# Performance work log

Hardware: AMD Instinct MI355X
Metric: run time of the kernel (lower is better)

## Reference

```python
import jax, jax.numpy as jnp
import numpy as np
from jax import lax

VOCAB = 32000
D = 256      # d_model
N = 16       # n_neurons
NL = 6       # n_layers
DS = 16      # d_state
DC = 4       # d_conv
DI = 512     # d_inner = expand * d_model
DTR = 16     # dt_rank = ceil(D/16)
NH = 4       # attention heads
HD = D // NH
B, L = 1, 128


def setup_inputs() -> dict:
    key = jax.random.key(0)
    ks = list(jax.random.split(key, 32))
    it = iter(ks)

    def rn(shape, scale):
        return jax.random.normal(next(it), shape, jnp.float32) * scale

    p = {}
    p["x"] = jax.random.randint(next(it), (B, L), 0, VOCAB, dtype=jnp.int32)
    p["embedding"] = rn((VOCAB, D), 0.02)
    p["norm1_w"] = jnp.ones((NL, D)); p["norm1_b"] = jnp.zeros((NL, D))
    p["norm2_w"] = jnp.ones((NL, D)); p["norm2_b"] = jnp.zeros((NL, D))
    # Mamba params (stacked over layers)
    p["in_proj_w"] = rn((NL, 2 * DI, D), D ** -0.5)
    p["conv_w"] = rn((NL, DI, DC), DC ** -0.5)
    p["conv_b"] = jnp.zeros((NL, DI))
    p["x_proj_w"] = rn((NL, DTR + 2 * DS, DI), DI ** -0.5)
    p["dt_proj_w"] = rn((NL, DI, DTR), DTR ** -0.5)
    dt0 = jax.random.uniform(next(it), (NL, DI), jnp.float32, 1e-3, 1e-1)
    p["dt_proj_b"] = jnp.log(jnp.expm1(dt0))  # inverse softplus init
    p["A_log"] = jnp.log(jnp.tile(jnp.arange(1.0, DS + 1.0, dtype=jnp.float32), (NL, DI, 1)))
    p["skip_D"] = jnp.ones((NL, DI))
    p["out_proj_w"] = rn((NL, D, DI), DI ** -0.5)
    # cross-neuron MHA params
    p["attn_in_w"] = rn((NL, 3 * D, D), D ** -0.5)
    p["attn_in_b"] = jnp.zeros((NL, 3 * D))
    p["attn_out_w"] = rn((NL, D, D), D ** -0.5)
    p["attn_out_b"] = jnp.zeros((NL, D))
    p["norm_f_w"] = jnp.ones((D,)); p["norm_f_b"] = jnp.zeros((D,))
    p["head_b"] = jnp.zeros((VOCAB,))
    return p


def _ln(x, w, b):
    m = x.mean(-1, keepdims=True)
    v = ((x - m) ** 2).mean(-1, keepdims=True)
    return (x - m) * lax.rsqrt(v + 1e-5) * w + b


def _mamba(x, ipw, cw, cb, xpw, dpw, dpb, alog, dskip, opw):
    # x: (BN, L, D)
    BN, Ls, _ = x.shape
    xz = x @ ipw.T                       # (BN, L, 2*DI)
    u, z = xz[..., :DI], xz[..., DI:]
    # depthwise causal conv1d, kernel DC, left-pad DC-1
    uc = lax.conv_general_dilated(
        u.swapaxes(1, 2), cw[:, None, :], (1,), [(DC - 1, 0)],
        dimension_numbers=("NCH", "OIH", "NCH"), feature_group_count=DI)
    u = jax.nn.silu(uc + cb[None, :, None]).swapaxes(1, 2)  # (BN, L, DI)
    xdbl = u @ xpw.T                     # (BN, L, DTR+2*DS)
    dt = jax.nn.softplus(xdbl[..., :DTR] @ dpw.T + dpb)     # (BN, L, DI)
    Bm = xdbl[..., DTR:DTR + DS]
    Cm = xdbl[..., DTR + DS:]
    A = -jnp.exp(alog)                   # (DI, DS)

    def step(h, ins):
        dt_t, b_t, c_t, u_t = ins        # (BN,DI) (BN,DS) (BN,DS) (BN,DI)
        h = jnp.exp(dt_t[..., None] * A) * h + (dt_t * u_t)[..., None] * b_t[:, None, :]
        return h, jnp.einsum("bds,bs->bd", h, c_t)

    h0 = jnp.zeros((BN, DI, DS), x.dtype)
    _, ys = lax.scan(step, h0, (dt.swapaxes(0, 1), Bm.swapaxes(0, 1),
                                Cm.swapaxes(0, 1), u.swapaxes(0, 1)))
    y = ys.swapaxes(0, 1) + u * dskip
    return (y * jax.nn.silu(z)) @ opw.T


def _mha(x, iw, ib, ow, ob):
    # x: (B*L, N, D); self-attention across neurons
    Bq, S, _ = x.shape
    qkv = x @ iw.T + ib
    q, k, v = jnp.split(qkv, 3, axis=-1)
    q = q.reshape(Bq, S, NH, HD); k = k.reshape(Bq, S, NH, HD); v = v.reshape(Bq, S, NH, HD)
    att = jax.nn.softmax(jnp.einsum("bqhd,bkhd->bhqk", q, k) / np.float32(np.sqrt(HD)), axis=-1)
    o = jnp.einsum("bhqk,bkhd->bqhd", att, v).reshape(Bq, S, D)
    return o @ ow.T + ob


def reference(x, embedding, norm1_w, norm1_b, norm2_w, norm2_b, in_proj_w, conv_w,
              conv_b, x_proj_w, dt_proj_w, dt_proj_b, A_log, skip_D, out_proj_w,
              attn_in_w, attn_in_b, attn_out_w, attn_out_b, norm_f_w, norm_f_b, head_b):
    Bb, Ll = x.shape
    h = embedding[x]                                             # (B, L, D)
    h = jnp.broadcast_to(h[:, None], (Bb, N, Ll, D)).reshape(Bb * N, Ll, D)
    for i in range(NL):
        h = h + _mamba(_ln(h, norm1_w[i], norm1_b[i]), in_proj_w[i], conv_w[i],
                       conv_b[i], x_proj_w[i], dt_proj_w[i], dt_proj_b[i],
                       A_log[i], skip_D[i], out_proj_w[i])
        xc = _ln(h, norm2_w[i], norm2_b[i]).reshape(Bb, N, Ll, D)
        xc = xc.transpose(0, 2, 1, 3).reshape(Bb * Ll, N, D)
        co = _mha(xc, attn_in_w[i], attn_in_b[i], attn_out_w[i], attn_out_b[i])
        h = h + co.reshape(Bb, Ll, N, D).transpose(0, 2, 1, 3).reshape(Bb * N, Ll, D)
    h = h.reshape(Bb, N, Ll, D).mean(axis=1)                     # avg over neurons
    return _ln(h, norm_f_w, norm_f_b) @ embedding.T + head_b     # tied head
```

## Files before the change

### kernel.cpp

```cpp
#include <hip/hip_runtime.h>

constexpr int SEQ    = 128;
constexpr int NVOCAB = 32000;

constexpr size_t O_HA = 0;
constexpr size_t O_HB = O_HA + (size_t)SEQ*256;
constexpr size_t O_U  = O_HB + (size_t)SEQ*256;
constexpr size_t O_DT = O_U  + (size_t)SEQ*512;
constexpr size_t O_ZS = O_DT + (size_t)SEQ*512;
constexpr size_t O_BC = O_ZS + (size_t)SEQ*512;
constexpr size_t O_YG = O_BC + (size_t)SEQ*32;
constexpr size_t O_AH = O_YG + (size_t)SEQ*512;
constexpr size_t O_WC = O_AH + (size_t)SEQ*256;
constexpr size_t O_BB = O_WC + (size_t)6*256*256;

__device__ __forceinline__ float wsum(float p) {
    #pragma unroll
    for (int m = 1; m < 64; m <<= 1) p += __shfl_xor(p, m);
    return p;
}
__device__ __forceinline__ float dot4(float4 a, float4 b) {
    return a.x*b.x + a.y*b.y + a.z*b.z + a.w*b.w;
}

__global__ __launch_bounds__(256) void combo_kernel(
    const float* __restrict__ aiw, const float* __restrict__ aib,
    const float* __restrict__ aow, const float* __restrict__ aob,
    float* __restrict__ wc, float* __restrict__ bc)
{
    const int l   = blockIdx.x >> 4;
    const int c0  = (blockIdx.x & 15) * 16;
    const int tid = threadIdx.x;
    const int c   = c0 + (tid >> 4);
    const int k0  = (tid & 15) * 16;
    const float* av = aiw + (size_t)l*768*256 + (size_t)512*256;
    const float* ab = aib + l*768 + 512;
    const float* ow = aow + (size_t)l*256*256;
    const float* ob = aob + l*256;

    float4 acc[4] = {};
    for (int j0 = 0; j0 < 256; j0 += 4) {
        float4 a4 = *(const float4*)&ow[(size_t)c*256 + j0];
        #pragma unroll
        for (int jj = 0; jj < 4; ++jj) {
            float aj = (&a4.x)[jj];
            const float* wrow = av + (size_t)(j0+jj)*256 + k0;
            #pragma unroll
            for (int q = 0; q < 4; ++q) {
                float4 w4 = *(const float4*)(wrow + q*4);
                acc[q].x += aj*w4.x; acc[q].y += aj*w4.y;
                acc[q].z += aj*w4.z; acc[q].w += aj*w4.w;
            }
        }
    }
    float* wout = wc + (size_t)l*256*256 + (size_t)c*256 + k0;
    #pragma unroll
    for (int q = 0; q < 4; ++q) *(float4*)(wout + q*4) = acc[q];

    if ((tid & 15) == 0) {
        float b = ob[c];
        for (int j0 = 0; j0 < 256; j0 += 4) {
            float4 a4 = *(const float4*)&ow[(size_t)c*256 + j0];
            float4 b4 = *(const float4*)&ab[j0];
            b += a4.x*b4.x + a4.y*b4.y + a4.z*b4.z + a4.w*b4.w;
        }
        bc[l*256 + c] = b;
    }
}

template<int MR, int KK, int S>
__device__ __forceinline__ void gemm3(
    const float* __restrict__ Wg, const float* __restrict__ A, int AS,
    float* __restrict__ dest, int DS,
    const float* __restrict__ addsrc, int ASS, const float* __restrict__ bias)
{
    constexpr int NST = KK / (4 * S);
    const int tid = threadIdx.x;
    const int tq  = tid & (S - 1);
    const int c0  = (tid / S) * 2;
    const float* Wp0 = Wg + (size_t)c0*KK + tq*4;
    const float* Wp1 = Wp0 + KK;

    float acc0[MR], acc1[MR];
    #pragma unroll
    for (int r = 0; r < MR; ++r) { acc0[r] = 0.f; acc1[r] = 0.f; }

    float4 wa0 = *(const float4*)(Wp0);
    float4 wa1 = *(const float4*)(Wp1);
    float4 wb0 = *(const float4*)(Wp0 + 4*S);
    float4 wb1 = *(const float4*)(Wp1 + 4*S);

    #pragma unroll 1
    for (int st = 0; st < NST; st += 2) {
        float4 na0, na1, nb0, nb1;
        const bool pa = (st + 2 < NST);
        const bool pb = (st + 3 < NST);
        if (pa) { na0 = *(const float4*)(Wp0 + (st+2)*4*S);
                  na1 = *(const float4*)(Wp1 + (st+2)*4*S); }
        if (pb) { nb0 = *(const float4*)(Wp0 + (st+3)*4*S);
                  nb1 = *(const float4*)(Wp1 + (st+3)*4*S); }
        const int k0 = st*4*S + tq*4;
        #pragma unroll
        for (int r = 0; r < MR; ++r) {
            float4 a = *(const float4*)&A[r*AS + k0];
            acc0[r] += dot4(a, wa0);
            acc1[r] += dot4(a, wa1);
        }
        const int k1 = k0 + 4*S;
        #pragma unroll
        for (int r = 0; r < MR; ++r) {
            float4 a = *(const float4*)&A[r*AS + k1];
            acc0[r] += dot4(a, wb0);
            acc1[r] += dot4(a, wb1);
        }
        if (pa) { wa0 = na0; wa1 = na1; }
        if (pb) { wb0 = nb0; wb1 = nb1; }
    }
    #pragma unroll
    for (int m = 1; m < S; m <<= 1) {
        #pragma unroll
        for (int r = 0; r < MR; ++r) {
            acc0[r] += __shfl_xor(acc0[r], m);
            acc1[r] += __shfl_xor(acc1[r], m);
        }
    }
    if (tq == 0) {
        #pragma unroll
        for (int r = 0; r < MR; ++r) {
            float ox = acc0[r], oy = acc1[r];
            if (bias) { ox += bias[c0]; oy += bias[c0+1]; }
            if (addsrc) {
                float2 s = *(const float2*)&addsrc[r*ASS + c0];
                ox += s.x; oy += s.y;
            }
            float2 o; o.x = ox; o.y = oy;
            *(float2*)&dest[r*DS + c0] = o;
        }
    }
}

__device__ __forceinline__ void ln_row(const float* __restrict__ src, float* __restrict__ dst,
                                       const float* __restrict__ w, const float* __restrict__ b)
{
    int lane = threadIdx.x & 63;
    float4 x = *(const float4*)&src[lane*4];
    float sm = wsum(x.x + x.y + x.z + x.w);
    float mean = sm * (1.0f/256.0f);
    float d0 = x.x-mean, d1 = x.y-mean, d2 = x.z-mean, d3 = x.w-mean;
    float var = wsum(d0*d0 + d1*d1 + d2*d2 + d3*d3) * (1.0f/256.0f);
    float rstd = rsqrtf(var + 1e-5f);
    float4 ww = *(const float4*)&w[lane*4];
    float4 bb = *(const float4*)&b[lane*4];
    float4 o;
    o.x = d0*rstd*ww.x + bb.x;
    o.y = d1*rstd*ww.y + bb.y;
    o.z = d2*rstd*ww.z + bb.z;
    o.w = d3*rstd*ww.w + bb.w;
    *(float4*)&dst[lane*4] = o;
}

__global__ __launch_bounds__(1024, 4) void rowk_kernel(
    const int* __restrict__ x, const float* __restrict__ emb,
    const float* __restrict__ n1w_l, const float* __restrict__ n1b_l,
    const float* __restrict__ n2w_l, const float* __restrict__ n2b_l,
    const float* __restrict__ ipw_l, const float* __restrict__ cw_l, const float* __restrict__ cb_l,
    const float* __restrict__ xpw_l, const float* __restrict__ dpw_l, const float* __restrict__ dpb_l,
    const float* __restrict__ opw_l, const float* __restrict__ wc_l, const float* __restrict__ bc_l,
    const float* __restrict__ nfw, const float* __restrict__ nfb,
    const float* __restrict__ hin, float* __restrict__ hout,
    const float* __restrict__ ygv, float* __restrict__ uv, float* __restrict__ dtv,
    float* __restrict__ zsv, float* __restrict__ bcv, float* __restrict__ AH,
    int li)
{
    __shared__ float SM[6336];
    float* hP  = SM;
    float* h1  = SM + 1056;
    float* sLN = SM + 2112;
    float* sAX = SM + 3168;
    float* zR  = SM + 5248;
    float* suR = SM + 5760;
    float* sxR = SM + 6272;

    const int r = blockIdx.x;
    const int tid = threadIdx.x;
    const int lane = tid & 63, wv = tid >> 6;
    int rr[4];
    #pragma unroll
    for (int j = 0; j < 4; ++j) { int v = r - 3 + j; rr[j] = v < 0 ? 0 : v; }

    {
        int hr = tid >> 8, hc = tid & 255;
        if (li <= 1) hP[hr*264 + hc] = emb[(size_t)x[rr[hr]]*256 + hc];
        else         hP[hr*264 + hc] = hin[rr[hr]*256 + hc];
    }
    if (li >= 1) {
        int yr = tid >> 9, yc = tid & 511;
        sAX[yr*520 + yc]     = ygv[rr[yr]*512 + yc];
        sAX[(2+yr)*520 + yc] = ygv[rr[2+yr]*512 + yc];
    }
    __syncthreads();

    float* hC = hP;
    if (li >= 1) {
        gemm3<4,512,8>(opw_l, sAX, 520, h1, 264, hP, 264, nullptr);
        __syncthreads();
        if (wv < 4) ln_row(h1 + wv*264, sLN + wv*264, n2w_l, n2b_l);
        __syncthreads();
        gemm3<4,256,8>(wc_l, sLN, 264, h1, 264, h1, 264, bc_l);
        __syncthreads();
        hC = h1;
        if (tid < 256) hout[r*256 + tid] = h1[3*264 + tid];
        if (li == 6) {
            if (tid < 256) {
                float v = h1[3*264 + tid];
                float s = wsum(v);
                float q = wsum(v*v);
                if (lane == 0) { sxR[wv] = s; sxR[8 + wv] = q; }
            }
            __syncthreads();
            if (tid < 256) {
                float v = h1[3*264 + tid];
                float mean = (sxR[0]+sxR[1]+sxR[2]+sxR[3]) * (1.0f/256.0f);
                float var  = (sxR[8]+sxR[9]+sxR[10]+sxR[11]) * (1.0f/256.0f) - mean*mean;
                float rstd = rsqrtf(var + 1e-5f);
                AH[r*256 + tid] = (v - mean)*rstd*nfw[tid] + nfb[tid];
            }
            return;
        }
    }

    if (wv < 4) ln_row(hC + wv*264, sLN + wv*264, n1w_l, n1b_l);
    __syncthreads();
    gemm3<4,256,4>(ipw_l,                   sLN,         264, sAX, 520, nullptr, 0, nullptr);
    gemm3<1,256,4>(ipw_l + (size_t)512*256, sLN + 3*264, 264, zR,  512, nullptr, 0, nullptr);
    __syncthreads();

    if (tid < 512) {
        int d = tid;
        float4 c4 = *(const float4*)&cw_l[d*4];
        float acc = cb_l[d];
        if (r >= 3) acc += sAX[d]        * c4.x;
        if (r >= 2) acc += sAX[520 + d]  * c4.y;
        if (r >= 1) acc += sAX[1040 + d] * c4.z;
        acc += sAX[1560 + d] * c4.w;
        float sg = acc / (1.0f + __expf(-acc));
        suR[d] = sg;
        uv[r*512 + d] = sg;
        float z = zR[d];
        zsv[r*512 + d] = z / (1.0f + __expf(-z));
    }
    __syncthreads();

    {
        float4 a0 = *(const float4*)&suR[lane*4];
        float4 a1 = *(const float4*)&suR[256 + lane*4];
        float p[3];
        #pragma unroll
        for (int j = 0; j < 3; ++j) {
            int c = wv*3 + j;
            float4 q0 = *(const float4*)&xpw_l[(size_t)c*512 + lane*4];
            float4 q1 = *(const float4*)&xpw_l[(size_t)c*512 + 256 + lane*4];
            p[j] = dot4(a0, q0) + dot4(a1, q1);
        }
        #pragma unroll
        for (int m = 1; m < 64; m <<= 1) {
            #pragma unroll
            for (int j = 0; j < 3; ++j) p[j] += __shfl_xor(p[j], m);
        }
        if (lane == 0) {
            #pragma unroll
            for (int j = 0; j < 3; ++j) sxR[wv*3 + j] = p[j];
        }
    }
    __syncthreads();
    if (tid >= 16 && tid < 48) bcv[r*32 + tid - 16] = sxR[tid];

    if (tid < 512) {
        int d = tid;
        float4 sx0 = *(const float4*)&sxR[0];
        float4 sx1 = *(const float4*)&sxR[4];
        float4 sx2 = *(const float4*)&sxR[8];
        float4 sx3 = *(const float4*)&sxR[12];
        const float4* dp = (const float4*)&dpw_l[(size_t)d*16];
        float acc = dpb_l[d] + dot4(dp[0], sx0) + dot4(dp[1], sx1)
                             + dot4(dp[2], sx2) + dot4(dp[3], sx3);
        dtv[r*512 + d] = fmaxf(acc, 0.0f) + log1pf(__expf(-fabsf(acc)));
    }
}

__global__ __launch_bounds__(64) void scan_kernel(
    const float* __restrict__ dt, const float* __restrict__ u, const float* __restrict__ zs,
    const float* __restrict__ bcv,
    const float* __restrict__ alog_l, const float* __restrict__ dsk_l,
    float* __restrict__ yg)
{
    __shared__ float sdt[4*132];
    __shared__ float su2[4*132];
    __shared__ float sz2[4*132];
    __shared__ float sB [16*132];
    __shared__ float sC [16*132];
    const int tid = threadIdx.x;
    const int s  = tid & 15;
    const int dl = tid >> 4;
    const int d0 = blockIdx.x * 4;
    const int d  = d0 + dl;

    #pragma unroll
    for (int tt = 0; tt < 2; ++tt) {
        const int t = tid + tt*64;
        float4 q;
        q = *(const float4*)&dt[t*512 + d0];
        sdt[0*132+t]=q.x; sdt[1*132+t]=q.y; sdt[2*132+t]=q.z; sdt[3*132+t]=q.w;
        q = *(const float4*)&u[t*512 + d0];
        su2[0*132+t]=q.x; su2[1*132+t]=q.y; su2[2*132+t]=q.z; su2[3*132+t]=q.w;
        q = *(const float4*)&zs[t*512 + d0];
        sz2[0*132+t]=q.x; sz2[1*132+t]=q.y; sz2[2*132+t]=q.z; sz2[3*132+t]=q.w;
        float4 b0 = *(const float4*)&bcv[t*32 + 0];
        float4 b1 = *(const float4*)&bcv[t*32 + 4];
        float4 b2 = *(const float4*)&bcv[t*32 + 8];
        float4 b3 = *(const float4*)&bcv[t*32 + 12];
        sB[ 0*132+t]=b0.x; sB[ 1*132+t]=b0.y; sB[ 2*132+t]=b0.z; sB[ 3*132+t]=b0.w;
        sB[ 4*132+t]=b1.x; sB[ 5*132+t]=b1.y; sB[ 6*132+t]=b1.z; sB[ 7*132+t]=b1.w;
        sB[ 8*132+t]=b2.x; sB[ 9*132+t]=b2.y; sB[10*132+t]=b2.z; sB[11*132+t]=b2.w;
        sB[12*132+t]=b3.x; sB[13*132+t]=b3.y; sB[14*132+t]=b3.z; sB[15*132+t]=b3.w;
        float4 c0 = *(const float4*)&bcv[t*32 + 16];
        float4 c1 = *(const float4*)&bcv[t*32 + 20];
        float4 c2 = *(const float4*)&bcv[t*32 + 24];
        float4 c3 = *(const float4*)&bcv[t*32 + 28];
        sC[ 0*132+t]=c0.x; sC[ 1*132+t]=c0.y; sC[ 2*132+t]=c0.z; sC[ 3*132+t]=c0.w;
        sC[ 4*132+t]=c1.x; sC[ 5*132+t]=c1.y; sC[ 6*132+t]=c1.z; sC[ 7*132+t]=c1.w;
        sC[ 8*132+t]=c2.x; sC[ 9*132+t]=c2.y; sC[10*132+t]=c2.z; sC[11*132+t]=c2.w;
        sC[12*132+t]=c3.x; sC[13*132+t]=c3.y; sC[14*132+t]=c3.z; sC[15*132+t]=c3.w;
    }
    __syncthreads();

    const float a_ds = -__expf(alog_l[d*16 + s]);
    const float dskv = dsk_l[d];
    float hst = 0.0f;
    #pragma unroll 8
    for (int t = 0; t < SEQ; ++t) {
        float dtvv = sdt[dl*132 + t];
        float uvv  = su2[dl*132 + t];
        hst = __expf(dtvv * a_ds) * hst + dtvv * uvv * sB[s*132 + t];
        float p = hst * sC[s*132 + t];
        p += __shfl_xor(p, 1);
        p += __shfl_xor(p, 2);
        p += __shfl_xor(p, 4);
        p += __shfl_xor(p, 8);
        if (s == 0) yg[t*512 + d] = (p + uvv * dskv) * sz2[dl*132 + t];
    }
}

__global__ __launch_bounds__(256) void head_kernel(
    const float* __restrict__ AH, const float* __restrict__ emb,
    const float* __restrict__ hb, float* __restrict__ out)
{
    __shared__ float sA[32*132];
    __shared__ float sW[32*68];
    const int tid = threadIdx.x;
    const int c0  = blockIdx.x * 64;
    const int ar = tid >> 1;
    const int ak = (tid & 1) * 16;
    const int wc = tid & 63;
    const int wk = (tid >> 6) * 8;
    const int rg = tid >> 4;
    const int cg = tid & 15;

    const float* Ap = AH  + (size_t)ar*256 + ak;
    const float* Wp = emb + (size_t)(c0 + wc)*256 + wk;

    float4 ra0 = *(const float4*)(Ap + 0);
    float4 ra1 = *(const float4*)(Ap + 4);
    float4 ra2 = *(const float4*)(Ap + 8);
    float4 ra3 = *(const float4*)(Ap + 12);
    float4 rw0 = *(const float4*)(Wp + 0);
    float4 rw1 = *(const float4*)(Wp + 4);

    float acc[8][4] = {};

    for (int kc = 0; kc < 256; kc += 32) {
        if (kc) __syncthreads();
        sA[(ak+ 0)*132+ar]=ra0.x; sA[(ak+ 1)*132+ar]=ra0.y; sA[(ak+ 2)*132+ar]=ra0.z; sA[(ak+ 3)*132+ar]=ra0.w;
        sA[(ak+ 4)*132+ar]=ra1.x; sA[(ak+ 5)*132+ar]=ra1.y; sA[(ak+ 6)*132+ar]=ra1.z; sA[(ak+ 7)*132+ar]=ra1.w;
        sA[(ak+ 8)*132+ar]=ra2.x; sA[(ak+ 9)*132+ar]=ra2.y; sA[(ak+10)*132+ar]=ra2.z; sA[(ak+11)*132+ar]=ra2.w;
        sA[(ak+12)*132+ar]=ra3.x; sA[(ak+13)*132+ar]=ra3.y; sA[(ak+14)*132+ar]=ra3.z; sA[(ak+15)*132+ar]=ra3.w;
        sW[(wk+0)*68+wc]=rw0.x; sW[(wk+1)*68+wc]=rw0.y; sW[(wk+2)*68+wc]=rw0.z; sW[(wk+3)*68+wc]=rw0.w;
        sW[(wk+4)*68+wc]=rw1.x; sW[(wk+5)*68+wc]=rw1.y; sW[(wk+6)*68+wc]=rw1.z; sW[(wk+7)*68+wc]=rw1.w;
        __syncthreads();
        if (kc + 32 < 256) {
            ra0 = *(const float4*)(Ap + kc + 32);
            ra1 = *(const float4*)(Ap + kc + 36);
            ra2 = *(const float4*)(Ap + kc + 40);
            ra3 = *(const float4*)(Ap + kc + 44);
            rw0 = *(const float4*)(Wp + kc + 32);
            rw1 = *(const float4*)(Wp + kc + 36);
        }
        #pragma unroll
        for (int k = 0; k < 32; ++k) {
            float4 a0 = *(const float4*)&sA[k*132 + rg*8];
            float4 a1 = *(const float4*)&sA[k*132 + rg*8 + 4];
            float4 b  = *(const float4*)&sW[k*68  + cg*4];
            float av[8] = {a0.x,a0.y,a0.z,a0.w, a1.x,a1.y,a1.z,a1.w};
            #pragma unroll
            for (int i = 0; i < 8; ++i) {
                acc[i][0] += av[i]*b.x;
                acc[i][1] += av[i]*b.y;
                acc[i][2] += av[i]*b.z;
                acc[i][3] += av[i]*b.w;
            }
        }
    }

    const int c = c0 + cg*4;
    float4 h4 = *(const float4*)&hb[c];
    #pragma unroll
    for (int i = 0; i < 8; ++i) {
        int r = rg*8 + i;
        float4 o;
        o.x = acc[i][0] + h4.x;
        o.y = acc[i][1] + h4.y;
        o.z = acc[i][2] + h4.z;
        o.w = acc[i][3] + h4.w;
        *(float4*)&out[(size_t)r*NVOCAB + c] = o;
    }
}

extern "C" void kernel_launch(void* const* d_in, const int* in_sizes, int n_in,
                              void* d_out, int out_size, void* d_ws, size_t ws_size,
                              hipStream_t stream)
{
    const int*   xin = (const int*)d_in[0];
    const float* emb = (const float*)d_in[1];
    const float* n1w = (const float*)d_in[2];
    const float* n1b = (const float*)d_in[3];
    const float* n2w = (const float*)d_in[4];
    const float* n2b = (const float*)d_in[5];
    const float* ipw = (const float*)d_in[6];
    const float* cw  = (const float*)d_in[7];
    const float* cb  = (const float*)d_in[8];
    const float* xpw = (const float*)d_in[9];
    const float* dpw = (const float*)d_in[10];
    const float* dpb = (const float*)d_in[11];
    const float* alog= (const float*)d_in[12];
    const float* dsk = (const float*)d_in[13];
    const float* opw = (const float*)d_in[14];
    const float* aiw = (const float*)d_in[15];
    const float* aib = (const float*)d_in[16];
    const float* aow = (const float*)d_in[17];
    const float* aob = (const float*)d_in[18];
    const float* nfw = (const float*)d_in[19];
    const float* nfb = (const float*)d_in[20];
    const float* hb  = (const float*)d_in[21];
    float* ws  = (float*)d_ws;
    float* out = (float*)d_out;

    combo_kernel<<<96, 256, 0, stream>>>(aiw, aib, aow, aob, ws + O_WC, ws + O_BB);

    for (int i = 0; i <= 6; ++i) {
        int ka = i <= 5 ? i : 5;
        int kc = i >= 1 ? i - 1 : 0;
        const float* hin  = (i % 2 == 0) ? ws + O_HA : ws + O_HB;
        float*       hout = (i % 2 == 0) ? ws + O_HB : ws + O_HA;
        rowk_kernel<<<128, 1024, 0, stream>>>(
            xin, emb,
            n1w + ka*256, n1b + ka*256,
            n2w + kc*256, n2b + kc*256,
            ipw + (size_t)ka*1024*256, cw + (size_t)ka*512*4, cb + ka*512,
            xpw + (size_t)ka*48*512, dpw + (size_t)ka*512*16, dpb + ka*512,
            opw + (size_t)kc*256*512,
            ws + O_WC + (size_t)kc*256*256, ws + O_BB + kc*256,
            nfw, nfb,
            hin, hout,
            ws + O_YG, ws + O_U, ws + O_DT, ws + O_ZS, ws + O_BC, ws + O_AH,
            i);
        if (i <= 5)
            scan_kernel<<<128, 64, 0, stream>>>(
                ws + O_DT, ws + O_U, ws + O_ZS, ws + O_BC,
                alog + (size_t)i*512*16, dsk + i*512, ws + O_YG);
    }
    head_kernel<<<NVOCAB/64, 256, 0, stream>>>(ws + O_AH, emb, hb, out);
}
```

Before: 596.6 us.

## Tile the attention weight-combination GEMM through shared memory with register prefetch

```diff
diff --git a/kernel.cpp b/kernel.cpp
--- a/kernel.cpp
+++ b/kernel.cpp
@@ -28,41 +28,72 @@
     const float* __restrict__ aow, const float* __restrict__ aob,
     float* __restrict__ wc, float* __restrict__ bc)
 {
-    const int l   = blockIdx.x >> 4;
-    const int c0  = (blockIdx.x & 15) * 16;
+    __shared__ float sA[32*68];
+    __shared__ float sB[32*68];
+    const int l  = blockIdx.x >> 4;
+    const int t  = blockIdx.x & 15;
+    const int r0 = (t >> 2) * 64;
+    const int n0 = (t & 3) * 64;
     const int tid = threadIdx.x;
-    const int c   = c0 + (tid >> 4);
-    const int k0  = (tid & 15) * 16;
+
     const float* av = aiw + (size_t)l*768*256 + (size_t)512*256;
     const float* ab = aib + l*768 + 512;
     const float* ow = aow + (size_t)l*256*256;
     const float* ob = aob + l*256;
 
-    float4 acc[4] = {};
-    for (int j0 = 0; j0 < 256; j0 += 4) {
-        float4 a4 = *(const float4*)&ow[(size_t)c*256 + j0];
-        #pragma unroll
-        for (int jj = 0; jj < 4; ++jj) {
-            float aj = (&a4.x)[jj];
-            const float* wrow = av + (size_t)(j0+jj)*256 + k0;
-            #pragma unroll
-            for (int q = 0; q < 4; ++q) {
-                float4 w4 = *(const float4*)(wrow + q*4);
-                acc[q].x += aj*w4.x; acc[q].y += aj*w4.y;
-                acc[q].z += aj*w4.z; acc[q].w += aj*w4.w;
-            }
-        }
-    }
-    float* wout = wc + (size_t)l*256*256 + (size_t)c*256 + k0;
-    #pragma unroll
-    for (int q = 0; q < 4; ++q) *(float4*)(wout + q*4) = acc[q];
-
-    if ((tid & 15) == 0) {
+    const int ar = tid & 63, ah = (tid >> 6) * 8;
+    const int bk = tid >> 3, bn = (tid & 7) * 8;
+    const float* Ap = ow + (size_t)(r0 + ar)*256 + ah;
+    const float* Bp = av + (size_t)bk*256 + n0 + bn;
+
+    const int rg = tid >> 4, cg = tid & 15;
+
+    float4 ra0 = *(const float4*)(Ap);
+    float4 ra1 = *(const float4*)(Ap + 4);
+    float4 rb0 = *(const float4*)(Bp);
+    float4 rb1 = *(const float4*)(Bp + 4);
+
+    float acc[4][4] = {};
+
+    for (int kc = 0; kc < 256; kc += 32) {
+        if (kc) __syncthreads();
+        sA[(ah+0)*68+ar]=ra0.x; sA[(ah+1)*68+ar]=ra0.y; sA[(ah+2)*68+ar]=ra0.z; sA[(ah+3)*68+ar]=ra0.w;
+        sA[(ah+4)*68+ar]=ra1.x; sA[(ah+5)*68+ar]=ra1.y; sA[(ah+6)*68+ar]=ra1.z; sA[(ah+7)*68+ar]=ra1.w;
+        *(float4*)&sB[bk*68+bn]   = rb0;
+        *(float4*)&sB[bk*68+bn+4] = rb1;
+        __syncthreads();
+        if (kc + 32 < 256) {
+            ra0 = *(const float4*)(Ap + kc + 32);
+            ra1 = *(const float4*)(Ap + kc + 36);
+            rb0 = *(const float4*)(Bp + (size_t)(kc + 32)*256);
+            rb1 = *(const float4*)(Bp + (size_t)(kc + 32)*256 + 4);
+        }
+        #pragma unroll
+        for (int k = 0; k < 32; ++k) {
+            float4 a = *(const float4*)&sA[k*68 + rg*4];
+            float4 b = *(const float4*)&sB[k*68 + cg*4];
+            acc[0][0] += a.x*b.x; acc[0][1] += a.x*b.y; acc[0][2] += a.x*b.z; acc[0][3] += a.x*b.w;
+            acc[1][0] += a.y*b.x; acc[1][1] += a.y*b.y; acc[1][2] += a.y*b.z; acc[1][3] += a.y*b.w;
+            acc[2][0] += a.z*b.x; acc[2][1] += a.z*b.y; acc[2][2] += a.z*b.z; acc[2][3] += a.z*b.w;
+            acc[3][0] += a.w*b.x; acc[3][1] += a.w*b.y; acc[3][2] += a.w*b.z; acc[3][3] += a.w*b.w;
+        }
+    }
+
+    float* wout = wc + (size_t)l*256*256;
+    #pragma unroll
+    for (int i = 0; i < 4; ++i) {
+        int row = r0 + rg*4 + i;
+        float4 o; o.x = acc[i][0]; o.y = acc[i][1]; o.z = acc[i][2]; o.w = acc[i][3];
+        *(float4*)&wout[(size_t)row*256 + n0 + cg*4] = o;
+    }
+
+    if (n0 == 0 && tid < 64) {
+        int c = r0 + tid;
         float b = ob[c];
         for (int j0 = 0; j0 < 256; j0 += 4) {
             float4 a4 = *(const float4*)&ow[(size_t)c*256 + j0];
             float4 b4 = *(const float4*)&ab[j0];
-            b += a4.x*b4.x + a4.y*b4.y + a4.z*b4.z + a4.w*b4.w;
+            b += dot4(a4, b4);
         }
         bc[l*256 + c] = b;
     }
```

Result: faster. 550.9 us (-7.7%).
